# Kernel optimization log

Hardware: AMD Instinct MI355X
Metric: run time of the kernel (lower is better)

The kernel has to match this reference:

```python
import jax, jax.numpy as jnp
import numpy as np

N = 100000
IN_F, HID, OUT = 256, 128, 64
NNZ = 1600000
EQ = 200000


def setup_inputs() -> dict:
    key = jax.random.key(0)
    ks = jax.random.split(key, 10)
    x = jax.random.normal(ks[0], (N, IN_F), dtype=jnp.float32)
    adj_rows = jnp.sort(jax.random.randint(ks[1], (NNZ,), 0, N, dtype=jnp.int32))
    adj_cols = jax.random.randint(ks[2], (NNZ,), 0, N, dtype=jnp.int32)
    adj_vals = jax.random.uniform(ks[3], (NNZ,), dtype=jnp.float32)
    edge_index = jax.random.randint(ks[4], (2, EQ), 0, N, dtype=jnp.int32)
    # params (torch Linear default init: U(-1/sqrt(fan_in), 1/sqrt(fan_in)))
    s1 = 1.0 / np.sqrt(IN_F)
    W1 = jax.random.uniform(ks[5], (IN_F, HID), minval=-s1, maxval=s1, dtype=jnp.float32)
    b1 = jax.random.uniform(ks[6], (HID,), minval=-s1, maxval=s1, dtype=jnp.float32)
    s2 = 1.0 / np.sqrt(HID)
    W2 = jax.random.uniform(ks[7], (HID, OUT), minval=-s2, maxval=s2, dtype=jnp.float32)
    b2 = jax.random.uniform(ks[8], (OUT,), minval=-s2, maxval=s2, dtype=jnp.float32)
    return {"x": x, "adj_rows": adj_rows, "adj_cols": adj_cols, "adj_vals": adj_vals,
            "edge_index": edge_index, "W1": W1, "b1": b1, "W2": W2, "b2": b2}


def spmm(rows, cols, vals, dense):
    # out[i,:] = sum_{e: rows[e]==i} vals[e] * dense[cols[e],:]
    msgs = vals[:, None] * dense[cols]  # [nnz, d]
    return jax.ops.segment_sum(msgs, rows, num_segments=N)


def reference(x, adj_rows, adj_cols, adj_vals, edge_index, W1, b1, W2, b2):
    # GCN layer 1: linear then sparse aggregation
    h = spmm(adj_rows, adj_cols, adj_vals, x @ W1 + b1)  # [N, HID]
    h = jax.nn.relu(h)  # dropout is identity in eval mode
    # GCN layer 2
    z = spmm(adj_rows, adj_cols, adj_vals, h @ W2 + b2)  # [N, OUT]
    # decode: gather src/dst embeddings, elementwise dot
    src, dst = edge_index[0], edge_index[1]
    return jnp.sum(z[src] * z[dst], axis=1)  # [EQ]
```

## Files before the change

### kernel.cpp

```cpp
#include <hip/hip_runtime.h>

constexpr int NN    = 100000;
constexpr int NNZ_E = 1600000;
constexpr int EQn   = 200000;
constexpr int INF_  = 256;
constexpr int HIDF  = 128;
constexpr int OUTF  = 64;

typedef float  f32x4  __attribute__((ext_vector_type(4)));
typedef short  bf16x8 __attribute__((ext_vector_type(8)));

__device__ inline unsigned short f2bf(float f) {
    union { float f; unsigned int i; } x; x.f = f;
    unsigned int r = x.i + 0x7fffu + ((x.i >> 16) & 1u);
    return (unsigned short)(r >> 16);
}

__device__ inline void gl2lds16(const void* g, void* l) {
    __builtin_amdgcn_global_load_lds(
        (const __attribute__((address_space(1))) void*)g,
        (__attribute__((address_space(3))) void*)l, 16, 0, 0);
}

__global__ __launch_bounds__(256) void build_row_ptr(const int* __restrict__ rows,
                                                     int* __restrict__ ptr) {
    int i = blockIdx.x * 256 + threadIdx.x;
    if (i > NN) return;
    int lo = 0, hi = NNZ_E;
    while (lo < hi) {
        int mid = (lo + hi) >> 1;
        if (rows[mid] < i) lo = mid + 1; else hi = mid;
    }
    ptr[i] = lo;
}

__global__ __launch_bounds__(256) void convert_weights(const float* __restrict__ W1,
                                                       const float* __restrict__ W2,
                                                       unsigned short* __restrict__ W1t,
                                                       unsigned short* __restrict__ W2t) {
    int i = blockIdx.x * 256 + threadIdx.x;
    if (i < INF_ * HIDF) {
        int k = i >> 7, n = i & 127;
        W1t[n * INF_ + k] = f2bf(W1[i]);
    }
    if (i < HIDF * OUTF) {
        int k = i >> 6, n = i & 63;
        W2t[n * HIDF + k] = f2bf(W2[i]);
    }
}

template<int K, int NCOLS, bool A_IS_BF16>
__global__ __launch_bounds__(256) void gemm_async(const void* __restrict__ Av,
                                                  const unsigned short* __restrict__ Bt,
                                                  const float* __restrict__ bias,
                                                  unsigned short* __restrict__ C,
                                                  int M) {
    constexpr int NT   = NCOLS / 16;
    constexpr int KS   = K / 32;
    constexpr int ABPR = A_IS_BF16 ? K * 2 : K * 4;
    constexpr int RPC  = 1024 / ABPR;
    constexpr int CPW  = 16 / RPC;
    constexpr int PADW = NCOLS + 8;
    constexpr int LDS_A  = 4 * CPW * 1040;
    constexpr int LDS_EP = 4 * 16 * PADW * 2;
    static_assert(LDS_EP <= LDS_A, "epilogue must fit in A buffer");
    __shared__ __align__(16) unsigned char lds8[LDS_A];

    const int tid  = threadIdx.x;
    const int wave = tid >> 6;
    const int lane = tid & 63;
    const int quad = lane >> 4;
    const int l16  = lane & 15;
    const int row0w = blockIdx.x * 64 + wave * 16;

    unsigned char* wbase = lds8 + wave * CPW * 1040;
    const char* abase = (const char*)Av;
    #pragma unroll
    for (int ch = 0; ch < CPW; ++ch) {
        int r0 = row0w + ch * RPC;
        if (r0 > M - RPC) r0 = M - RPC;
        gl2lds16(abase + (size_t)r0 * ABPR + lane * 16, wbase + ch * 1040);
    }
    __syncthreads();

    f32x4 acc[NT];
    #pragma unroll
    for (int t = 0; t < NT; ++t) acc[t] = (f32x4){0.f, 0.f, 0.f, 0.f};

    const unsigned short* bp = &Bt[(size_t)l16 * K + quad * 8];
    #pragma unroll
    for (int ks = 0; ks < KS; ++ks) {
        bf16x8 af;
        if constexpr (A_IS_BF16) {
            int flat = l16 * ABPR + ks * 64 + quad * 16;
            af = *(const bf16x8*)(wbase + (flat >> 10) * 1040 + (flat & 1023));
        } else {
            int flat = l16 * ABPR + ks * 128 + quad * 32;
            const unsigned char* p = wbase + (flat >> 10) * 1040 + (flat & 1023);
            float4 a0 = *(const float4*)p;
            float4 a1 = *(const float4*)(p + 16);
            af[0] = (short)f2bf(a0.x); af[1] = (short)f2bf(a0.y);
            af[2] = (short)f2bf(a0.z); af[3] = (short)f2bf(a0.w);
            af[4] = (short)f2bf(a1.x); af[5] = (short)f2bf(a1.y);
            af[6] = (short)f2bf(a1.z); af[7] = (short)f2bf(a1.w);
        }
        #pragma unroll
        for (int t = 0; t < NT; ++t) {
            bf16x8 bf = *(const bf16x8*)(bp + (size_t)t * 16 * K + ks * 32);
            acc[t] = __builtin_amdgcn_mfma_f32_16x16x32_bf16(af, bf, acc[t], 0, 0, 0);
        }
    }

    __syncthreads();
    unsigned short* cst = (unsigned short*)lds8;
    unsigned short* my = &cst[wave * 16 * PADW];
    #pragma unroll
    for (int t = 0; t < NT; ++t) {
        const float bb = bias[t * 16 + l16];
        #pragma unroll
        for (int r = 0; r < 4; ++r)
            my[(quad * 4 + r) * PADW + t * 16 + l16] = f2bf(acc[t][r] + bb);
    }
    __syncthreads();
    constexpr int CH = NCOLS / 8;
    #pragma unroll
    for (int i = 0; i < (16 * CH) / 64; ++i) {
        int id = i * 64 + lane;
        int r  = id / CH, cc = id % CH;
        int grow = blockIdx.x * 64 + wave * 16 + r;
        if (grow < M)
            *(uint4*)&C[(size_t)grow * NCOLS + cc * 8] =
                *(const uint4*)&my[r * PADW + cc * 8];
    }
}

__device__ inline void fma8_bf16(float* acc, uint4 q, float v) {
    union { unsigned int i; float f; } t;
    #pragma unroll
    for (int p = 0; p < 4; ++p) {
        unsigned int w = (&q.x)[p];
        t.i = w << 16;          acc[2*p]   += v * t.f;
        t.i = w & 0xffff0000u;  acc[2*p+1] += v * t.f;
    }
}

template<int D, bool RELU>
__global__ __launch_bounds__(256) void spmm_bf16(const int* __restrict__ ptr,
                                                 const int* __restrict__ cols,
                                                 const float* __restrict__ vals,
                                                 const unsigned short* __restrict__ dense,
                                                 unsigned short* __restrict__ outm) {
    constexpr int LPR = D / 8;
    constexpr int RPB = 256 / LPR;
    const int lane = threadIdx.x % LPR;
    const int row  = blockIdx.x * RPB + threadIdx.x / LPR;
    if (row >= NN) return;

    int e = ptr[row];
    const int e1 = ptr[row + 1];
    const size_t lo8 = (size_t)lane * 8;
    float acc[8] = {};

    for (; e + 4 <= e1; e += 4) {
        int   c0 = cols[e],   c1 = cols[e+1], c2 = cols[e+2], c3 = cols[e+3];
        float v0 = vals[e],   v1 = vals[e+1], v2 = vals[e+2], v3 = vals[e+3];
        uint4 q0 = *(const uint4*)&dense[(size_t)c0 * D + lo8];
        uint4 q1 = *(const uint4*)&dense[(size_t)c1 * D + lo8];
        uint4 q2 = *(const uint4*)&dense[(size_t)c2 * D + lo8];
        uint4 q3 = *(const uint4*)&dense[(size_t)c3 * D + lo8];
        fma8_bf16(acc, q0, v0);
        fma8_bf16(acc, q1, v1);
        fma8_bf16(acc, q2, v2);
        fma8_bf16(acc, q3, v3);
    }
    for (; e < e1; ++e) {
        int   c = cols[e];
        float v = vals[e];
        uint4 q = *(const uint4*)&dense[(size_t)c * D + lo8];
        fma8_bf16(acc, q, v);
    }

    if (RELU) {
        #pragma unroll
        for (int p = 0; p < 8; ++p) acc[p] = fmaxf(acc[p], 0.f);
    }
    uint4 o;
    #pragma unroll
    for (int p = 0; p < 4; ++p)
        (&o.x)[p] = (unsigned int)f2bf(acc[2*p]) | ((unsigned int)f2bf(acc[2*p+1]) << 16);
    *(uint4*)&outm[(size_t)row * D + lo8] = o;
}

__global__ __launch_bounds__(256) void decode_dot_bf16(const unsigned short* __restrict__ z,
                                                       const int* __restrict__ ei,
                                                       float* __restrict__ outv) {
    const int lane = threadIdx.x & 7;
    const int e    = blockIdx.x * 32 + (threadIdx.x >> 3);
    if (e >= EQn) return;
    const int s = ei[e];
    const int d = ei[EQn + e];
    uint4 qa = *(const uint4*)&z[(size_t)s * 64 + lane * 8];
    uint4 qb = *(const uint4*)&z[(size_t)d * 64 + lane * 8];
    union { unsigned int i; float f; } ta, tb;
    float p = 0.f;
    #pragma unroll
    for (int k = 0; k < 4; ++k) {
        unsigned int wa = (&qa.x)[k], wb = (&qb.x)[k];
        ta.i = wa << 16;         tb.i = wb << 16;         p += ta.f * tb.f;
        ta.i = wa & 0xffff0000u; tb.i = wb & 0xffff0000u; p += ta.f * tb.f;
    }
    p += __shfl_xor(p, 1, 8);
    p += __shfl_xor(p, 2, 8);
    p += __shfl_xor(p, 4, 8);
    if (lane == 0) outv[e] = p;
}

extern "C" void kernel_launch(void* const* d_in, const int* in_sizes, int n_in,
                              void* d_out, int out_size, void* d_ws, size_t ws_size,
                              hipStream_t stream) {
    (void)in_sizes; (void)n_in; (void)out_size; (void)ws_size;

    const float* x        = (const float*)d_in[0];
    const int*   adj_rows = (const int*)  d_in[1];
    const int*   adj_cols = (const int*)  d_in[2];
    const float* adj_vals = (const float*)d_in[3];
    const int*   ei       = (const int*)  d_in[4];
    const float* W1       = (const float*)d_in[5];
    const float* b1       = (const float*)d_in[6];
    const float* W2       = (const float*)d_in[7];
    const float* b2       = (const float*)d_in[8];
    float* out = (float*)d_out;

    char* ws = (char*)d_ws;
    int* row_ptr = (int*)ws;
    size_t off = ((size_t)(NN + 1) * sizeof(int) + 511) & ~(size_t)511;
    unsigned short* W1t = (unsigned short*)(ws + off);
    unsigned short* W2t = W1t + (size_t)HIDF * INF_;
    unsigned short* slotA = W2t + (size_t)OUTF * HIDF;
    slotA = (unsigned short*)(((size_t)slotA + 511) & ~(size_t)511);
    unsigned short* slotB = slotA + (size_t)NN * HIDF;

    build_row_ptr<<<(NN + 256) / 256, 256, 0, stream>>>(adj_rows, row_ptr);
    convert_weights<<<(INF_ * HIDF + 255) / 256, 256, 0, stream>>>(W1, W2, W1t, W2t);

    gemm_async<INF_, HIDF, false><<<(NN + 63) / 64, 256, 0, stream>>>(
        x, W1t, b1, slotA, NN);

    spmm_bf16<HIDF, true><<<(NN + 15) / 16, 256, 0, stream>>>(
        row_ptr, adj_cols, adj_vals, slotA, slotB);

    gemm_async<HIDF, OUTF, true><<<(NN + 63) / 64, 256, 0, stream>>>(
        slotB, W2t, b2, slotA, NN);

    spmm_bf16<OUTF, false><<<(NN + 31) / 32, 256, 0, stream>>>(
        row_ptr, adj_cols, adj_vals, slotA, slotB);

    decode_dot_bf16<<<EQn / 32, 256, 0, stream>>>(slotB, ei, out);
}
```

Measured before the change: 349.9 us.

## Replace per-tile GEMM with persistent double-buffered kernel staging weights in LDS

Rewrites both dense GEMMs as persistent kernels with fixed grids of 512-thread blocks. Each block loads the bf16 weight matrix into padded LDS once, then loops over row tiles. It prefetches the next A tile into a second LDS buffer while computing the current one. The aim is to cut repeated global weight reads and launch/tail overhead and to overlap A loads with MFMA work. In exchange, occupancy drops to one block per CU under a large LDS footprint, and throughput now depends on the grid-size choice.

```diff
diff --git a/kernel.cpp b/kernel.cpp
--- a/kernel.cpp
+++ b/kernel.cpp
@@ -49,88 +49,115 @@
     }
 }
 
-template<int K, int NCOLS, bool A_IS_BF16>
-__global__ __launch_bounds__(256) void gemm_async(const void* __restrict__ Av,
-                                                  const unsigned short* __restrict__ Bt,
-                                                  const float* __restrict__ bias,
-                                                  unsigned short* __restrict__ C,
-                                                  int M) {
-    constexpr int NT   = NCOLS / 16;
+template<int K, int NCOLS, int TR, int CGB, bool A_IS_BF16>
+__global__ __launch_bounds__(512, 1) void gemm_persist(const void* __restrict__ Av,
+                                                       const unsigned short* __restrict__ Bt,
+                                                       const float* __restrict__ bias,
+                                                       unsigned short* __restrict__ C,
+                                                       int M) {
     constexpr int KS   = K / 32;
+    constexpr int NT   = 2;
+    constexpr int CG   = 1 << CGB;
+    constexpr int RB   = 8 / CG;
+    static_assert(RB * 16 == TR, "tile rows = 16*RB");
+    static_assert(CG * 32 == NCOLS, "cols = 32*CG");
     constexpr int ABPR = A_IS_BF16 ? K * 2 : K * 4;
     constexpr int RPC  = 1024 / ABPR;
-    constexpr int CPW  = 16 / RPC;
+    constexpr int NCH  = TR / RPC;
+    constexpr int CPWW = NCH / 8;
+    constexpr int ABUF = NCH * 1040;
+    constexpr int PK   = K + 8;
     constexpr int PADW = NCOLS + 8;
-    constexpr int LDS_A  = 4 * CPW * 1040;
-    constexpr int LDS_EP = 4 * 16 * PADW * 2;
-    static_assert(LDS_EP <= LDS_A, "epilogue must fit in A buffer");
-    __shared__ __align__(16) unsigned char lds8[LDS_A];
+    constexpr int BSB  = NCOLS * PK * 2;
+    constexpr int EPB  = TR * PADW * 2;
+    static_assert(TR * NCOLS / 8 == 512, "one uint4 store per thread");
+    __shared__ __align__(16) unsigned char smem[2 * ABUF + BSB + EPB];
+    unsigned char*  Ab = smem;
+    unsigned short* Bs = (unsigned short*)(smem + 2 * ABUF);
+    unsigned short* ep = (unsigned short*)(smem + 2 * ABUF + BSB);
 
     const int tid  = threadIdx.x;
     const int wave = tid >> 6;
     const int lane = tid & 63;
     const int quad = lane >> 4;
     const int l16  = lane & 15;
-    const int row0w = blockIdx.x * 64 + wave * 16;
-
-    unsigned char* wbase = lds8 + wave * CPW * 1040;
+    const int cg   = wave & (CG - 1);
+    const int rb   = wave >> CGB;
+
+    for (int i = tid; i < NCOLS * K / 8; i += 512) {
+        int n = i / (K / 8), kc = (i % (K / 8)) * 8;
+        *(uint4*)&Bs[n * PK + kc] = *(const uint4*)&Bt[(size_t)n * K + kc];
+    }
+
+    const int ntiles = (M + TR - 1) / TR;
     const char* abase = (const char*)Av;
-    #pragma unroll
-    for (int ch = 0; ch < CPW; ++ch) {
-        int r0 = row0w + ch * RPC;
-        if (r0 > M - RPC) r0 = M - RPC;
-        gl2lds16(abase + (size_t)r0 * ABPR + lane * 16, wbase + ch * 1040);
-    }
-    __syncthreads();
-
-    f32x4 acc[NT];
-    #pragma unroll
-    for (int t = 0; t < NT; ++t) acc[t] = (f32x4){0.f, 0.f, 0.f, 0.f};
-
-    const unsigned short* bp = &Bt[(size_t)l16 * K + quad * 8];
-    #pragma unroll
-    for (int ks = 0; ks < KS; ++ks) {
-        bf16x8 af;
-        if constexpr (A_IS_BF16) {
-            int flat = l16 * ABPR + ks * 64 + quad * 16;
-            af = *(const bf16x8*)(wbase + (flat >> 10) * 1040 + (flat & 1023));
-        } else {
-            int flat = l16 * ABPR + ks * 128 + quad * 32;
-            const unsigned char* p = wbase + (flat >> 10) * 1040 + (flat & 1023);
-            float4 a0 = *(const float4*)p;
-            float4 a1 = *(const float4*)(p + 16);
-            af[0] = (short)f2bf(a0.x); af[1] = (short)f2bf(a0.y);
-            af[2] = (short)f2bf(a0.z); af[3] = (short)f2bf(a0.w);
-            af[4] = (short)f2bf(a1.x); af[5] = (short)f2bf(a1.y);
-            af[6] = (short)f2bf(a1.z); af[7] = (short)f2bf(a1.w);
-        }
-        #pragma unroll
-        for (int t = 0; t < NT; ++t) {
-            bf16x8 bf = *(const bf16x8*)(bp + (size_t)t * 16 * K + ks * 32);
-            acc[t] = __builtin_amdgcn_mfma_f32_16x16x32_bf16(af, bf, acc[t], 0, 0, 0);
-        }
-    }
-
-    __syncthreads();
-    unsigned short* cst = (unsigned short*)lds8;
-    unsigned short* my = &cst[wave * 16 * PADW];
-    #pragma unroll
-    for (int t = 0; t < NT; ++t) {
-        const float bb = bias[t * 16 + l16];
-        #pragma unroll
-        for (int r = 0; r < 4; ++r)
-            my[(quad * 4 + r) * PADW + t * 16 + l16] = f2bf(acc[t][r] + bb);
-    }
-    __syncthreads();
-    constexpr int CH = NCOLS / 8;
-    #pragma unroll
-    for (int i = 0; i < (16 * CH) / 64; ++i) {
-        int id = i * 64 + lane;
-        int r  = id / CH, cc = id % CH;
-        int grow = blockIdx.x * 64 + wave * 16 + r;
-        if (grow < M)
-            *(uint4*)&C[(size_t)grow * NCOLS + cc * 8] =
-                *(const uint4*)&my[r * PADW + cc * 8];
+
+    auto stage = [&](int b, int tile0) {
+        unsigned char* dst = Ab + b * ABUF;
+        #pragma unroll
+        for (int j = 0; j < CPWW; ++j) {
+            int ch = wave * CPWW + j;
+            int r0 = tile0 + ch * RPC;
+            if (r0 > M - RPC) r0 = M - RPC;
+            gl2lds16(abase + (size_t)r0 * ABPR + lane * 16, dst + ch * 1040);
+        }
+    };
+
+    int t = blockIdx.x, buf = 0;
+    if (t < ntiles) stage(0, t * TR);
+
+    for (; t < ntiles; t += gridDim.x) {
+        __syncthreads();
+        int tn = t + gridDim.x;
+        if (tn < ntiles) stage(1 - buf, tn * TR);
+
+        const unsigned char* ab = Ab + buf * ABUF;
+        const int arow = rb * 16 + l16;
+        f32x4 acc[NT];
+        #pragma unroll
+        for (int tt = 0; tt < NT; ++tt) acc[tt] = (f32x4){0.f, 0.f, 0.f, 0.f};
+
+        #pragma unroll
+        for (int ks = 0; ks < KS; ++ks) {
+            bf16x8 af;
+            if constexpr (A_IS_BF16) {
+                int flat = arow * ABPR + ks * 64 + quad * 16;
+                af = *(const bf16x8*)(ab + (flat >> 10) * 1040 + (flat & 1023));
+            } else {
+                int flat = arow * ABPR + ks * 128 + quad * 32;
+                const unsigned char* p = ab + (flat >> 10) * 1040 + (flat & 1023);
+                float4 a0 = *(const float4*)p;
+                float4 a1 = *(const float4*)(p + 16);
+                af[0] = (short)f2bf(a0.x); af[1] = (short)f2bf(a0.y);
+                af[2] = (short)f2bf(a0.z); af[3] = (short)f2bf(a0.w);
+                af[4] = (short)f2bf(a1.x); af[5] = (short)f2bf(a1.y);
+                af[6] = (short)f2bf(a1.z); af[7] = (short)f2bf(a1.w);
+            }
+            #pragma unroll
+            for (int tt = 0; tt < NT; ++tt) {
+                bf16x8 bfr = *(const bf16x8*)&Bs[(cg * 32 + tt * 16 + l16) * PK + ks * 32 + quad * 8];
+                acc[tt] = __builtin_amdgcn_mfma_f32_16x16x32_bf16(af, bfr, acc[tt], 0, 0, 0);
+            }
+        }
+
+        #pragma unroll
+        for (int tt = 0; tt < NT; ++tt) {
+            const int col = cg * 32 + tt * 16 + l16;
+            const float bb = bias[col];
+            #pragma unroll
+            for (int r = 0; r < 4; ++r)
+                ep[(rb * 16 + quad * 4 + r) * PADW + col] = f2bf(acc[tt][r] + bb);
+        }
+        __syncthreads();
+        {
+            constexpr int CH = NCOLS / 8;
+            int r = tid / CH, cc = tid % CH;
+            int grow = t * TR + r;
+            if (grow < M)
+                *(uint4*)&C[(size_t)grow * NCOLS + cc * 8] =
+                    *(const uint4*)&ep[r * PADW + cc * 8];
+        }
+        buf ^= 1;
     }
 }
 
@@ -243,13 +270,13 @@
     build_row_ptr<<<(NN + 256) / 256, 256, 0, stream>>>(adj_rows, row_ptr);
     convert_weights<<<(INF_ * HIDF + 255) / 256, 256, 0, stream>>>(W1, W2, W1t, W2t);
 
-    gemm_async<INF_, HIDF, false><<<(NN + 63) / 64, 256, 0, stream>>>(
+    gemm_persist<INF_, HIDF, 32, 2, false><<<256, 512, 0, stream>>>(
         x, W1t, b1, slotA, NN);
 
     spmm_bf16<HIDF, true><<<(NN + 15) / 16, 256, 0, stream>>>(
         row_ptr, adj_cols, adj_vals, slotA, slotB);
 
-    gemm_async<HIDF, OUTF, true><<<(NN + 63) / 64, 256, 0, stream>>>(
+    gemm_persist<HIDF, OUTF, 64, 1, true><<<512, 512, 0, stream>>>(
         slotB, W2t, b2, slotA, NN);
 
     spmm_bf16<OUTF, false><<<(NN + 31) / 32, 256, 0, stream>>>(
```

Measured after the change: 300.8 us. 14.0% less time.
